# Performance work log

Hardware: AMD Instinct MI355X
Metric: run time of the kernel (lower is better)

Reference implementation:

```python
import jax, jax.numpy as jnp
import numpy as np

N_NODES = 100000
N_EDGES = 1600000
F_IN = 128
F_OUT = 32
HEADS = 8
ALPHA = 0.2  # LeakyReLU slope


def setup_inputs() -> dict:
    key = jax.random.key(0)
    ks = jax.random.split(key, 7)
    x = jax.random.normal(ks[0], (N_NODES, F_IN), dtype=jnp.float32)
    row = jnp.sort(jax.random.randint(ks[1], (N_EDGES,), 0, N_NODES, dtype=jnp.int32))
    col = jax.random.randint(ks[2], (N_EDGES,), 0, N_NODES, dtype=jnp.int32)
    kernels = jax.random.normal(ks[3], (HEADS, F_IN, F_OUT), dtype=jnp.float32) * 0.1
    att_self = jax.random.normal(ks[4], (HEADS, F_OUT), dtype=jnp.float32) * 0.1
    att_neigh = jax.random.normal(ks[5], (HEADS, F_OUT), dtype=jnp.float32) * 0.1
    biases = jax.random.normal(ks[6], (HEADS, F_OUT), dtype=jnp.float32) * 0.1
    return {"x": x, "row": row, "col": col, "kernels": kernels,
            "att_self": att_self, "att_neigh": att_neigh, "biases": biases}


def reference(x, row, col, kernels, att_self, att_neigh, biases):
    # GraphAttention (GAT), eval mode (dropout inactive), concat over heads.
    N = x.shape[0]
    outs = []
    for h in range(kernels.shape[0]):  # fixed small head loop
        feat = x @ kernels[h]                     # [N, F_OUT]
        a_s = feat @ att_self[h]                  # [N]
        a_n = feat @ att_neigh[h]                 # [N]
        e = a_s[row] + a_n[col]                   # [E] edge logits (SDDMM)
        e = jnp.where(e > 0, e, ALPHA * e)        # LeakyReLU(0.2)
        # row-wise (destination-node) sparse softmax, numerically stable
        m = jax.ops.segment_max(e, row, num_segments=N)
        ex = jnp.exp(e - m[row])
        denom = jax.ops.segment_sum(ex, row, num_segments=N)
        alpha = ex / denom[row]                   # [E]
        # SpMM: out[i] = sum_{e: row[e]=i} alpha[e] * feat[col[e]]
        msg = alpha[:, None] * feat[col]          # [E, F_OUT]
        out = jax.ops.segment_sum(msg, row, num_segments=N) + biases[h]
        outs.append(out)
    return jnp.concatenate(outs, axis=1)          # [N, HEADS*F_OUT]
```

## Files before the change

### kernel.cpp

```cpp
#include <hip/hip_runtime.h>
#include <hip/hip_bf16.h>
#include <math.h>


#define F_IN   128
#define F_ALL  256
#define HEADS  8
#define F_OUT  32
#define ALPHA  0.2f

using f32x4  = __attribute__((ext_vector_type(4))) float;
using bf16x8 = __attribute__((ext_vector_type(8))) short;
using u16x8  = __attribute__((ext_vector_type(8))) unsigned short;

static __device__ __forceinline__ unsigned short f32_to_bf16(float f) {
  union { float f; unsigned u; } v; v.f = f;
  unsigned r = v.u + 0x7FFF + ((v.u >> 16) & 1);
  return (unsigned short)(r >> 16);
}
static __device__ __forceinline__ unsigned cvt_pk_bf16(float lo, float hi) {
  unsigned r;
  asm("v_cvt_pk_bf16_f32 %0, %1, %2" : "=v"(r) : "v"(lo), "v"(hi));
  return r;
}
static __device__ __forceinline__ float bf16_lo(unsigned d) {
  return __uint_as_float(d << 16);
}
static __device__ __forceinline__ float bf16_hi(unsigned d) {
  return __uint_as_float(d & 0xffff0000u);
}

__global__ __launch_bounds__(256) void prep(const float* __restrict__ x,
                                            const float* __restrict__ kern,
                                            const float* __restrict__ att_s,
                                            const float* __restrict__ att_n,
                                            const int* __restrict__ row,
                                            unsigned short* __restrict__ xb,
                                            unsigned short* __restrict__ Wt,
                                            float* __restrict__ ws,
                                            float* __restrict__ wn,
                                            int* __restrict__ ptr,
                                            int total_x8, int N, int E) {
  int id = blockIdx.x * 256 + threadIdx.x;
  if (id < total_x8) {
    const float4* x4 = reinterpret_cast<const float4*>(x);
    float4 v0 = x4[(size_t)id * 2], v1 = x4[(size_t)id * 2 + 1];
    u16x8 o;
    o[0] = f32_to_bf16(v0.x); o[1] = f32_to_bf16(v0.y);
    o[2] = f32_to_bf16(v0.z); o[3] = f32_to_bf16(v0.w);
    o[4] = f32_to_bf16(v1.x); o[5] = f32_to_bf16(v1.y);
    o[6] = f32_to_bf16(v1.z); o[7] = f32_to_bf16(v1.w);
    *reinterpret_cast<u16x8*>(xb + (size_t)id * 8) = o;
  }
  if (id < F_ALL * F_IN) {
    int c = id >> 7, k = id & 127;
    Wt[id] = f32_to_bf16(kern[(size_t)(c >> 5) * (F_IN * F_OUT) + k * F_OUT + (c & 31)]);
  }
  if (id < 2 * HEADS * F_IN) {
    int which = id >> 10;
    int hk = id & 1023;
    int h = hk >> 7, k = hk & 127;
    const float* att = which ? att_n : att_s;
    float s = 0.f;
#pragma unroll
    for (int f = 0; f < F_OUT; ++f)
      s += kern[(size_t)h * (F_IN * F_OUT) + k * F_OUT + f] * att[h * F_OUT + f];
    (which ? wn : ws)[hk] = s;
  }
  if (id <= N) {
    int lo = 0, hi = E;
    while (lo < hi) {
      int mid = (lo + hi) >> 1;
      if (row[mid] < id) lo = mid + 1; else hi = mid;
    }
    ptr[id] = lo;
  }
}

__global__ __launch_bounds__(256) void gemm_aproj(
    const unsigned short* __restrict__ xb,
    const unsigned short* __restrict__ Wt,
    const float* __restrict__ x,
    const float* __restrict__ ws, const float* __restrict__ wn,
    unsigned short* __restrict__ featb,
    float* __restrict__ a_s, float* __restrict__ a_n,
    int N, int gemm_blocks, int aproj_waves) {
  const int t = threadIdx.x;

  if ((int)blockIdx.x < gemm_blocks) {
    const int w  = t >> 6;
    const int l  = t & 63;
    const int lr = l & 15;
    const int lq = l >> 4;
    const int n0 = blockIdx.x * 64 + w * 16;

    f32x4 acc[16];
#pragma unroll
    for (int ct = 0; ct < 16; ++ct) acc[ct] = (f32x4){0.f, 0.f, 0.f, 0.f};

    int ar = n0 + lr; if (ar >= N) ar = N - 1;
    const unsigned short* xrow = xb + (size_t)ar * F_IN + lq * 8;
    bf16x8 xfr[4];
#pragma unroll
    for (int kc = 0; kc < 4; ++kc)
      xfr[kc] = *reinterpret_cast<const bf16x8*>(xrow + kc * 32);

#pragma unroll
    for (int ct = 0; ct < 16; ++ct) {
      const unsigned short* wrow = Wt + (size_t)(ct * 16 + lr) * F_IN + lq * 8;
#pragma unroll
      for (int kc = 0; kc < 4; ++kc) {
        bf16x8 wfr = *reinterpret_cast<const bf16x8*>(wrow + kc * 32);
        acc[ct] = __builtin_amdgcn_mfma_f32_16x16x32_bf16(wfr, xfr[kc], acc[ct], 0, 0, 0);
      }
    }
    if (n0 + lr < N) {
      unsigned short* frow = featb + (size_t)ar * F_ALL + lq * 4;
#pragma unroll
      for (int ct = 0; ct < 16; ++ct) {
        uint2 v;
        v.x = cvt_pk_bf16(acc[ct][0], acc[ct][1]);
        v.y = cvt_pk_bf16(acc[ct][2], acc[ct][3]);
        *reinterpret_cast<uint2*>(frow + ct * 16) = v;
      }
    }
    return;
  }

  const int l = t & 63;
  const int o = l & 15, q = l >> 4;
  const int wid = (((int)blockIdx.x - gemm_blocks) * 256 + t) >> 6;

  const float* wrow = (o < 8 ? ws + o * F_IN : wn + (o - 8) * F_IN) + q * 32;
  float4 wv[8];
#pragma unroll
  for (int i = 0; i < 8; i++) wv[i] = reinterpret_cast<const float4*>(wrow)[i];

  for (int n = wid; n < N; n += aproj_waves) {
    const float4* xr = reinterpret_cast<const float4*>(x + (size_t)n * F_IN + q * 32);
    float acc = 0.f;
#pragma unroll
    for (int i = 0; i < 8; i++) {
      float4 xv = xr[i];
      acc += xv.x * wv[i].x + xv.y * wv[i].y + xv.z * wv[i].z + xv.w * wv[i].w;
    }
    acc += __shfl_xor(acc, 16);
    acc += __shfl_xor(acc, 32);
    if (l < 16) {
      if (o < 8) a_s[n * HEADS + o] = acc;
      else       a_n[n * HEADS + (o - 8)] = acc;
    }
  }
}

__global__ __launch_bounds__(256) void gat_scatter(
    const unsigned short* __restrict__ featb,
    const float* __restrict__ a_s, const float* __restrict__ a_n,
    const int* __restrict__ col, const int* __restrict__ ptr,
    const float* __restrict__ biases, float* __restrict__ out, int N) {
  const int t    = threadIdx.x;
  const int n    = blockIdx.x * 2 + (t >> 7);
  if (n >= N) return;
  const int tl   = t & 127;
  const int q    = tl & 15;
  const int h    = ((tl >> 5) << 1) | ((tl >> 4) & 1);
  const int obase = h * F_OUT + q * 2;

  const int start = ptr[n];
  const int deg   = ptr[n + 1] - start;

  const float2 bv = *reinterpret_cast<const float2*>(&biases[obase]);
  if (deg == 0) {
    *reinterpret_cast<float2*>(&out[(size_t)n * F_ALL + obase]) = bv;
    return;
  }

  const float as = a_s[n * HEADS + h];
  const unsigned* fu32 = reinterpret_cast<const unsigned*>(featb);
  const int dbase = h * 16 + q;

  if (deg <= 32) {
    int c1 = 0, c2 = 0;
    float ex1 = 0.f, ex2 = 0.f;
    if (q < deg) {
      c1 = col[start + q];
      float v = as + a_n[c1 * HEADS + h];
      v = v > 0.f ? v : ALPHA * v;
      ex1 = __expf(v);
    }
    if (q + 16 < deg) {
      c2 = col[start + q + 16];
      float v = as + a_n[c2 * HEADS + h];
      v = v > 0.f ? v : ALPHA * v;
      ex2 = __expf(v);
    }
    float sm = ex1 + ex2;
#pragma unroll
    for (int m = 1; m <= 8; m <<= 1) sm += __shfl_xor(sm, m);
    const float inv = 1.0f / sm;

    float a0 = 0.f, a1 = 0.f, b0 = 0.f, b1 = 0.f;
    const int d1 = ((deg < 16 ? deg : 16) + 1) & ~1;
    for (int e = 0; e < d1; e += 2) {
      int   ca = __shfl(c1,  e,     16);
      float wa = __shfl(ex1, e,     16);
      int   cb = __shfl(c1,  e + 1, 16);
      float wb = __shfl(ex1, e + 1, 16);
      unsigned da = fu32[(size_t)ca * 128 + dbase];
      unsigned db = fu32[(size_t)cb * 128 + dbase];
      a0 = fmaf(wa, bf16_lo(da), a0);
      a1 = fmaf(wa, bf16_hi(da), a1);
      b0 = fmaf(wb, bf16_lo(db), b0);
      b1 = fmaf(wb, bf16_hi(db), b1);
    }
    if (deg > 16) {
      const int d2 = (deg - 16 + 1) & ~1;
      for (int e = 0; e < d2; e += 2) {
        int   ca = __shfl(c2,  e,     16);
        float wa = __shfl(ex2, e,     16);
        int   cb = __shfl(c2,  e + 1, 16);
        float wb = __shfl(ex2, e + 1, 16);
        unsigned da = fu32[(size_t)ca * 128 + dbase];
        unsigned db = fu32[(size_t)cb * 128 + dbase];
        a0 = fmaf(wa, bf16_lo(da), a0);
        a1 = fmaf(wa, bf16_hi(da), a1);
        b0 = fmaf(wb, bf16_lo(db), b0);
        b1 = fmaf(wb, bf16_hi(db), b1);
      }
    }
    float2 o;
    o.x = (a0 + b0) * inv + bv.x;
    o.y = (a1 + b1) * inv + bv.y;
    *reinterpret_cast<float2*>(&out[(size_t)n * F_ALL + obase]) = o;
    return;
  }

  float sm = 0.f;
  for (int e = q; e < deg; e += 16) {
    int c = col[start + e];
    float v = as + a_n[c * HEADS + h];
    v = v > 0.f ? v : ALPHA * v;
    sm += __expf(v);
  }
#pragma unroll
  for (int m = 1; m <= 8; m <<= 1) sm += __shfl_xor(sm, m);
  const float inv = 1.0f / sm;

  float f0 = 0.f, f1 = 0.f;
  for (int e = 0; e < deg; ++e) {
    int c = col[start + e];
    float v = as + a_n[c * HEADS + h];
    v = v > 0.f ? v : ALPHA * v;
    float wv = __expf(v);
    unsigned d = fu32[(size_t)c * 128 + dbase];
    f0 = fmaf(wv, bf16_lo(d), f0);
    f1 = fmaf(wv, bf16_hi(d), f1);
  }
  float2 o;
  o.x = f0 * inv + bv.x;
  o.y = f1 * inv + bv.y;
  *reinterpret_cast<float2*>(&out[(size_t)n * F_ALL + obase]) = o;
}

extern "C" void kernel_launch(void* const* d_in, const int* in_sizes, int n_in,
                              void* d_out, int out_size, void* d_ws, size_t ws_size,
                              hipStream_t stream) {
  const float* x      = (const float*)d_in[0];
  const int*   row    = (const int*)d_in[1];
  const int*   col    = (const int*)d_in[2];
  const float* kern   = (const float*)d_in[3];
  const float* att_s  = (const float*)d_in[4];
  const float* att_n  = (const float*)d_in[5];
  const float* biases = (const float*)d_in[6];

  const int N = in_sizes[0] / F_IN;
  const int E = in_sizes[1];

  unsigned short* featb = (unsigned short*)d_ws;
  unsigned short* xb    = featb + (size_t)N * F_ALL;
  unsigned short* Wt    = xb + (size_t)N * F_IN;
  float* ws  = (float*)(Wt + F_ALL * F_IN);
  float* wn  = ws + HEADS * F_IN;
  float* a_s = wn + HEADS * F_IN;
  float* a_n = a_s + (size_t)N * HEADS;
  int*   ptr = (int*)(a_n + (size_t)N * HEADS);
  float* out = (float*)d_out;

  const int total_x8    = N * F_IN / 8;
  const int gemm_blocks = (N + 63) / 64;
  const int aproj_blocks = 1024;
  const int aproj_waves  = aproj_blocks * 4;

  hipLaunchKernelGGL(prep, dim3((total_x8 + 255) / 256), dim3(256), 0, stream,
                     x, kern, att_s, att_n, row, xb, Wt, ws, wn, ptr, total_x8, N, E);
  hipLaunchKernelGGL(gemm_aproj, dim3(gemm_blocks + aproj_blocks), dim3(256), 0, stream,
                     xb, Wt, x, ws, wn, featb, a_s, a_n, N, gemm_blocks, aproj_waves);
  hipLaunchKernelGGL(gat_scatter, dim3((N + 1) / 2), dim3(256), 0, stream,
                     featb, a_s, a_n, col, ptr, biases, out, N);
}
```

Before: 277.2 us.

## Fuse bf16 conversion of x into attention projection and widen scatter gathers

The prep kernel is split in two. A tiny prep0 builds the transposed bf16 weights and the folded attention vectors. prep1 computes the CSR pointers and the a_s/a_n projections, and writes the bf16 copy of x from the same registers, so x is read from memory once instead of twice. The MFMA feature GEMM becomes its own kernel that runs after this pass, which adds one launch and removes the overlap the combined gemm_aproj kernel had. In the scatter kernel each lane now gathers 4 bf16 features (8 bytes) per edge, two edges are processed in parallel per 16-lane group, and partial sums are combined with a shuffle before a float4 store.

New measurement: 577.1 us. +108.1%, slower.

```diff
diff --git a/kernel.cpp b/kernel.cpp
--- a/kernel.cpp
+++ b/kernel.cpp
@@ -11,7 +11,6 @@
 
 using f32x4  = __attribute__((ext_vector_type(4))) float;
 using bf16x8 = __attribute__((ext_vector_type(8))) short;
-using u16x8  = __attribute__((ext_vector_type(8))) unsigned short;
 
 static __device__ __forceinline__ unsigned short f32_to_bf16(float f) {
   union { float f; unsigned u; } v; v.f = f;
@@ -30,32 +29,13 @@
   return __uint_as_float(d & 0xffff0000u);
 }
 
-__global__ __launch_bounds__(256) void prep(const float* __restrict__ x,
-                                            const float* __restrict__ kern,
-                                            const float* __restrict__ att_s,
-                                            const float* __restrict__ att_n,
-                                            const int* __restrict__ row,
-                                            unsigned short* __restrict__ xb,
-                                            unsigned short* __restrict__ Wt,
-                                            float* __restrict__ ws,
-                                            float* __restrict__ wn,
-                                            int* __restrict__ ptr,
-                                            int total_x8, int N, int E) {
+__global__ __launch_bounds__(256) void prep0(const float* __restrict__ kern,
+                                             const float* __restrict__ att_s,
+                                             const float* __restrict__ att_n,
+                                             unsigned short* __restrict__ Wt,
+                                             float* __restrict__ ws,
+                                             float* __restrict__ wn) {
   int id = blockIdx.x * 256 + threadIdx.x;
-  if (id < total_x8) {
-    const float4* x4 = reinterpret_cast<const float4*>(x);
-    float4 v0 = x4[(size_t)id * 2], v1 = x4[(size_t)id * 2 + 1];
-    u16x8 o;
-    o[0] = f32_to_bf16(v0.x); o[1] = f32_to_bf16(v0.y);
-    o[2] = f32_to_bf16(v0.z); o[3] = f32_to_bf16(v0.w);
-    o[4] = f32_to_bf16(v1.x); o[5] = f32_to_bf16(v1.y);
-    o[6] = f32_to_bf16(v1.z); o[7] = f32_to_bf16(v1.w);
-    *reinterpret_cast<u16x8*>(xb + (size_t)id * 8) = o;
-  }
-  if (id < F_ALL * F_IN) {
-    int c = id >> 7, k = id & 127;
-    Wt[id] = f32_to_bf16(kern[(size_t)(c >> 5) * (F_IN * F_OUT) + k * F_OUT + (c & 31)]);
-  }
   if (id < 2 * HEADS * F_IN) {
     int which = id >> 10;
     int hk = id & 1023;
@@ -66,83 +46,54 @@
     for (int f = 0; f < F_OUT; ++f)
       s += kern[(size_t)h * (F_IN * F_OUT) + k * F_OUT + f] * att[h * F_OUT + f];
     (which ? wn : ws)[hk] = s;
-  }
-  if (id <= N) {
+  } else if (id < 4096) {
+    int base = (id - 2048) * 16;
+#pragma unroll
+    for (int i = base; i < base + 16; ++i) {
+      int c = i >> 7, k = i & 127;
+      Wt[i] = f32_to_bf16(kern[(size_t)(c >> 5) * (F_IN * F_OUT) + k * F_OUT + (c & 31)]);
+    }
+  }
+}
+
+__global__ __launch_bounds__(256) void prep1(const float* __restrict__ x,
+                                             const float* __restrict__ ws,
+                                             const float* __restrict__ wn,
+                                             const int* __restrict__ row,
+                                             unsigned short* __restrict__ xb,
+                                             float* __restrict__ a_s,
+                                             float* __restrict__ a_n,
+                                             int* __restrict__ ptr,
+                                             int N, int E) {
+  const int t   = threadIdx.x;
+  const int gid = blockIdx.x * 256 + t;
+  if (gid <= N) {
     int lo = 0, hi = E;
     while (lo < hi) {
       int mid = (lo + hi) >> 1;
-      if (row[mid] < id) lo = mid + 1; else hi = mid;
-    }
-    ptr[id] = lo;
-  }
-}
-
-__global__ __launch_bounds__(256) void gemm_aproj(
-    const unsigned short* __restrict__ xb,
-    const unsigned short* __restrict__ Wt,
-    const float* __restrict__ x,
-    const float* __restrict__ ws, const float* __restrict__ wn,
-    unsigned short* __restrict__ featb,
-    float* __restrict__ a_s, float* __restrict__ a_n,
-    int N, int gemm_blocks, int aproj_waves) {
-  const int t = threadIdx.x;
-
-  if ((int)blockIdx.x < gemm_blocks) {
-    const int w  = t >> 6;
-    const int l  = t & 63;
-    const int lr = l & 15;
-    const int lq = l >> 4;
-    const int n0 = blockIdx.x * 64 + w * 16;
-
-    f32x4 acc[16];
-#pragma unroll
-    for (int ct = 0; ct < 16; ++ct) acc[ct] = (f32x4){0.f, 0.f, 0.f, 0.f};
-
-    int ar = n0 + lr; if (ar >= N) ar = N - 1;
-    const unsigned short* xrow = xb + (size_t)ar * F_IN + lq * 8;
-    bf16x8 xfr[4];
-#pragma unroll
-    for (int kc = 0; kc < 4; ++kc)
-      xfr[kc] = *reinterpret_cast<const bf16x8*>(xrow + kc * 32);
-
-#pragma unroll
-    for (int ct = 0; ct < 16; ++ct) {
-      const unsigned short* wrow = Wt + (size_t)(ct * 16 + lr) * F_IN + lq * 8;
-#pragma unroll
-      for (int kc = 0; kc < 4; ++kc) {
-        bf16x8 wfr = *reinterpret_cast<const bf16x8*>(wrow + kc * 32);
-        acc[ct] = __builtin_amdgcn_mfma_f32_16x16x32_bf16(wfr, xfr[kc], acc[ct], 0, 0, 0);
-      }
-    }
-    if (n0 + lr < N) {
-      unsigned short* frow = featb + (size_t)ar * F_ALL + lq * 4;
-#pragma unroll
-      for (int ct = 0; ct < 16; ++ct) {
-        uint2 v;
-        v.x = cvt_pk_bf16(acc[ct][0], acc[ct][1]);
-        v.y = cvt_pk_bf16(acc[ct][2], acc[ct][3]);
-        *reinterpret_cast<uint2*>(frow + ct * 16) = v;
-      }
-    }
-    return;
+      if (row[mid] < gid) lo = mid + 1; else hi = mid;
+    }
+    ptr[gid] = lo;
   }
 
   const int l = t & 63;
   const int o = l & 15, q = l >> 4;
-  const int wid = (((int)blockIdx.x - gemm_blocks) * 256 + t) >> 6;
+  const int wid = gid >> 6;
+  const int nw  = (gridDim.x * 256) >> 6;
 
   const float* wrow = (o < 8 ? ws + o * F_IN : wn + (o - 8) * F_IN) + q * 32;
   float4 wv[8];
 #pragma unroll
   for (int i = 0; i < 8; i++) wv[i] = reinterpret_cast<const float4*>(wrow)[i];
 
-  for (int n = wid; n < N; n += aproj_waves) {
+  for (int n = wid; n < N; n += nw) {
     const float4* xr = reinterpret_cast<const float4*>(x + (size_t)n * F_IN + q * 32);
+    float4 xv[8];
     float acc = 0.f;
 #pragma unroll
     for (int i = 0; i < 8; i++) {
-      float4 xv = xr[i];
-      acc += xv.x * wv[i].x + xv.y * wv[i].y + xv.z * wv[i].z + xv.w * wv[i].w;
+      xv[i] = xr[i];
+      acc += xv[i].x * wv[i].x + xv[i].y * wv[i].y + xv[i].z * wv[i].z + xv[i].w * wv[i].w;
     }
     acc += __shfl_xor(acc, 16);
     acc += __shfl_xor(acc, 32);
@@ -150,6 +101,58 @@
       if (o < 8) a_s[n * HEADS + o] = acc;
       else       a_n[n * HEADS + (o - 8)] = acc;
     }
+    if (o < 4) {
+      uint4 pk;
+      pk.x = cvt_pk_bf16(xv[o * 2].x, xv[o * 2].y);
+      pk.y = cvt_pk_bf16(xv[o * 2].z, xv[o * 2].w);
+      pk.z = cvt_pk_bf16(xv[o * 2 + 1].x, xv[o * 2 + 1].y);
+      pk.w = cvt_pk_bf16(xv[o * 2 + 1].z, xv[o * 2 + 1].w);
+      *reinterpret_cast<uint4*>(xb + (size_t)n * F_IN + q * 32 + o * 8) = pk;
+    }
+  }
+}
+
+__global__ __launch_bounds__(256) void feat_gemm_mfma(
+    const unsigned short* __restrict__ xb,
+    const unsigned short* __restrict__ Wt,
+    unsigned short* __restrict__ featb,
+    int N) {
+  const int t  = threadIdx.x;
+  const int w  = t >> 6;
+  const int l  = t & 63;
+  const int lr = l & 15;
+  const int lq = l >> 4;
+  const int n0 = blockIdx.x * 64 + w * 16;
+
+  f32x4 acc[16];
+#pragma unroll
+  for (int ct = 0; ct < 16; ++ct) acc[ct] = (f32x4){0.f, 0.f, 0.f, 0.f};
+
+  int ar = n0 + lr; if (ar >= N) ar = N - 1;
+  const unsigned short* xrow = xb + (size_t)ar * F_IN + lq * 8;
+  bf16x8 xfr[4];
+#pragma unroll
+  for (int kc = 0; kc < 4; ++kc)
+    xfr[kc] = *reinterpret_cast<const bf16x8*>(xrow + kc * 32);
+
+#pragma unroll
+  for (int ct = 0; ct < 16; ++ct) {
+    const unsigned short* wrow = Wt + (size_t)(ct * 16 + lr) * F_IN + lq * 8;
+#pragma unroll
+    for (int kc = 0; kc < 4; ++kc) {
+      bf16x8 wfr = *reinterpret_cast<const bf16x8*>(wrow + kc * 32);
+      acc[ct] = __builtin_amdgcn_mfma_f32_16x16x32_bf16(wfr, xfr[kc], acc[ct], 0, 0, 0);
+    }
+  }
+  if (n0 + lr < N) {
+    unsigned short* frow = featb + (size_t)ar * F_ALL + lq * 4;
+#pragma unroll
+    for (int ct = 0; ct < 16; ++ct) {
+      uint2 v;
+      v.x = cvt_pk_bf16(acc[ct][0], acc[ct][1]);
+      v.y = cvt_pk_bf16(acc[ct][2], acc[ct][3]);
+      *reinterpret_cast<uint2*>(frow + ct * 16) = v;
+    }
   }
 }
 
@@ -158,38 +161,43 @@
     const float* __restrict__ a_s, const float* __restrict__ a_n,
     const int* __restrict__ col, const int* __restrict__ ptr,
     const float* __restrict__ biases, float* __restrict__ out, int N) {
-  const int t    = threadIdx.x;
-  const int n    = blockIdx.x * 2 + (t >> 7);
+  const int t  = threadIdx.x;
+  const int n  = blockIdx.x * 2 + (t >> 7);
   if (n >= N) return;
-  const int tl   = t & 127;
-  const int q    = tl & 15;
-  const int h    = ((tl >> 5) << 1) | ((tl >> 4) & 1);
-  const int obase = h * F_OUT + q * 2;
+  const int tl = t & 127;
+  const int g  = tl >> 5;
+  const int hh = (tl >> 4) & 1;
+  const int h  = g * 2 + hh;
+  const int s  = tl & 15;
+  const int p  = s >> 3;
+  const int q  = s & 7;
+  const int obase = h * F_OUT + q * 4;
 
   const int start = ptr[n];
   const int deg   = ptr[n + 1] - start;
 
-  const float2 bv = *reinterpret_cast<const float2*>(&biases[obase]);
   if (deg == 0) {
-    *reinterpret_cast<float2*>(&out[(size_t)n * F_ALL + obase]) = bv;
+    if (p == 0)
+      *reinterpret_cast<float4*>(&out[(size_t)n * F_ALL + obase]) =
+          *reinterpret_cast<const float4*>(&biases[obase]);
     return;
   }
 
   const float as = a_s[n * HEADS + h];
   const unsigned* fu32 = reinterpret_cast<const unsigned*>(featb);
-  const int dbase = h * 16 + q;
+  const size_t dbase = (size_t)h * 16 + q * 2;
 
   if (deg <= 32) {
     int c1 = 0, c2 = 0;
     float ex1 = 0.f, ex2 = 0.f;
-    if (q < deg) {
-      c1 = col[start + q];
+    if (s < deg) {
+      c1 = col[start + s];
       float v = as + a_n[c1 * HEADS + h];
       v = v > 0.f ? v : ALPHA * v;
       ex1 = __expf(v);
     }
-    if (q + 16 < deg) {
-      c2 = col[start + q + 16];
+    if (s + 16 < deg) {
+      c2 = col[start + s + 16];
       float v = as + a_n[c2 * HEADS + h];
       v = v > 0.f ? v : ALPHA * v;
       ex2 = __expf(v);
@@ -199,44 +207,43 @@
     for (int m = 1; m <= 8; m <<= 1) sm += __shfl_xor(sm, m);
     const float inv = 1.0f / sm;
 
-    float a0 = 0.f, a1 = 0.f, b0 = 0.f, b1 = 0.f;
+    float a0 = 0.f, a1 = 0.f, a2 = 0.f, a3 = 0.f;
     const int d1 = ((deg < 16 ? deg : 16) + 1) & ~1;
     for (int e = 0; e < d1; e += 2) {
-      int   ca = __shfl(c1,  e,     16);
-      float wa = __shfl(ex1, e,     16);
-      int   cb = __shfl(c1,  e + 1, 16);
-      float wb = __shfl(ex1, e + 1, 16);
-      unsigned da = fu32[(size_t)ca * 128 + dbase];
-      unsigned db = fu32[(size_t)cb * 128 + dbase];
-      a0 = fmaf(wa, bf16_lo(da), a0);
-      a1 = fmaf(wa, bf16_hi(da), a1);
-      b0 = fmaf(wb, bf16_lo(db), b0);
-      b1 = fmaf(wb, bf16_hi(db), b1);
+      int   c = __shfl(c1,  e + p, 16);
+      float w = __shfl(ex1, e + p, 16);
+      uint2 d = *reinterpret_cast<const uint2*>(fu32 + (size_t)c * 128 + dbase);
+      a0 = fmaf(w, bf16_lo(d.x), a0);
+      a1 = fmaf(w, bf16_hi(d.x), a1);
+      a2 = fmaf(w, bf16_lo(d.y), a2);
+      a3 = fmaf(w, bf16_hi(d.y), a3);
     }
     if (deg > 16) {
       const int d2 = (deg - 16 + 1) & ~1;
       for (int e = 0; e < d2; e += 2) {
-        int   ca = __shfl(c2,  e,     16);
-        float wa = __shfl(ex2, e,     16);
-        int   cb = __shfl(c2,  e + 1, 16);
-        float wb = __shfl(ex2, e + 1, 16);
-        unsigned da = fu32[(size_t)ca * 128 + dbase];
-        unsigned db = fu32[(size_t)cb * 128 + dbase];
-        a0 = fmaf(wa, bf16_lo(da), a0);
-        a1 = fmaf(wa, bf16_hi(da), a1);
-        b0 = fmaf(wb, bf16_lo(db), b0);
-        b1 = fmaf(wb, bf16_hi(db), b1);
+        int   c = __shfl(c2,  e + p, 16);
+        float w = __shfl(ex2, e + p, 16);
+        uint2 d = *reinterpret_cast<const uint2*>(fu32 + (size_t)c * 128 + dbase);
+        a0 = fmaf(w, bf16_lo(d.x), a0);
+        a1 = fmaf(w, bf16_hi(d.x), a1);
+        a2 = fmaf(w, bf16_lo(d.y), a2);
+        a3 = fmaf(w, bf16_hi(d.y), a3);
       }
     }
-    float2 o;
-    o.x = (a0 + b0) * inv + bv.x;
-    o.y = (a1 + b1) * inv + bv.y;
-    *reinterpret_cast<float2*>(&out[(size_t)n * F_ALL + obase]) = o;
+    a0 += __shfl_xor(a0, 8);
+    a1 += __shfl_xor(a1, 8);
+    a2 += __shfl_xor(a2, 8);
+    a3 += __shfl_xor(a3, 8);
+    if (p == 0) {
+      const float4 bv = *reinterpret_cast<const float4*>(&biases[obase]);
+      float4 o = {a0 * inv + bv.x, a1 * inv + bv.y, a2 * inv + bv.z, a3 * inv + bv.w};
+      *reinterpret_cast<float4*>(&out[(size_t)n * F_ALL + obase]) = o;
+    }
     return;
   }
 
   float sm = 0.f;
-  for (int e = q; e < deg; e += 16) {
+  for (int e = s; e < deg; e += 16) {
     int c = col[start + e];
     float v = as + a_n[c * HEADS + h];
     v = v > 0.f ? v : ALPHA * v;
@@ -246,20 +253,27 @@
   for (int m = 1; m <= 8; m <<= 1) sm += __shfl_xor(sm, m);
   const float inv = 1.0f / sm;
 
-  float f0 = 0.f, f1 = 0.f;
-  for (int e = 0; e < deg; ++e) {
+  float a0 = 0.f, a1 = 0.f, a2 = 0.f, a3 = 0.f;
+  for (int e = p; e < deg; e += 2) {
     int c = col[start + e];
     float v = as + a_n[c * HEADS + h];
     v = v > 0.f ? v : ALPHA * v;
-    float wv = __expf(v);
-    unsigned d = fu32[(size_t)c * 128 + dbase];
-    f0 = fmaf(wv, bf16_lo(d), f0);
-    f1 = fmaf(wv, bf16_hi(d), f1);
-  }
-  float2 o;
-  o.x = f0 * inv + bv.x;
-  o.y = f1 * inv + bv.y;
-  *reinterpret_cast<float2*>(&out[(size_t)n * F_ALL + obase]) = o;
+    float w = __expf(v);
+    uint2 d = *reinterpret_cast<const uint2*>(fu32 + (size_t)c * 128 + dbase);
+    a0 = fmaf(w, bf16_lo(d.x), a0);
+    a1 = fmaf(w, bf16_hi(d.x), a1);
+    a2 = fmaf(w, bf16_lo(d.y), a2);
+    a3 = fmaf(w, bf16_hi(d.y), a3);
+  }
+  a0 += __shfl_xor(a0, 8);
+  a1 += __shfl_xor(a1, 8);
+  a2 += __shfl_xor(a2, 8);
+  a3 += __shfl_xor(a3, 8);
+  if (p == 0) {
+    const float4 bv = *reinterpret_cast<const float4*>(&biases[obase]);
+    float4 o = {a0 * inv + bv.x, a1 * inv + bv.y, a2 * inv + bv.z, a3 * inv + bv.w};
+    *reinterpret_cast<float4*>(&out[(size_t)n * F_ALL + obase]) = o;
+  }
 }
 
 extern "C" void kernel_launch(void* const* d_in, const int* in_sizes, int n_in,
@@ -286,15 +300,12 @@
   int*   ptr = (int*)(a_n + (size_t)N * HEADS);
   float* out = (float*)d_out;
 
-  const int total_x8    = N * F_IN / 8;
-  const int gemm_blocks = (N + 63) / 64;
-  const int aproj_blocks = 1024;
-  const int aproj_waves  = aproj_blocks * 4;
-
-  hipLaunchKernelGGL(prep, dim3((total_x8 + 255) / 256), dim3(256), 0, stream,
-                     x, kern, att_s, att_n, row, xb, Wt, ws, wn, ptr, total_x8, N, E);
-  hipLaunchKernelGGL(gemm_aproj, dim3(gemm_blocks + aproj_blocks), dim3(256), 0, stream,
-                     xb, Wt, x, ws, wn, featb, a_s, a_n, N, gemm_blocks, aproj_waves);
+  hipLaunchKernelGGL(prep0, dim3(16), dim3(256), 0, stream,
+                     kern, att_s, att_n, Wt, ws, wn);
+  hipLaunchKernelGGL(prep1, dim3(2048), dim3(256), 0, stream,
+                     x, ws, wn, row, xb, a_s, a_n, ptr, N, E);
+  hipLaunchKernelGGL(feat_gemm_mfma, dim3((N + 63) / 64), dim3(256), 0, stream,
+                     xb, Wt, featb, N);
   hipLaunchKernelGGL(gat_scatter, dim3((N + 1) / 2), dim3(256), 0, stream,
                      featb, a_s, a_n, col, ptr, biases, out, N);
 }
```
